# Performance work log

Hardware: AMD Instinct MI355X
Metric: run time of the kernel (lower is better)

Reference implementation:

```python
import jax, jax.numpy as jnp
import numpy as np

N_QUBITS = 16
N_LAYERS = 4
BATCH = 512


def _apply_ry(state, theta, q, n):
    # state: [B, 2^n] real (RY/CNOT circuit from |0> stays real).
    # Wire 0 is the most-significant bit (PennyLane default.qubit ordering).
    B = state.shape[0]
    pre, post = 2 ** q, 2 ** (n - q - 1)
    s = state.reshape(B, pre, 2, post)
    half = jnp.reshape(theta, (-1,)) * 0.5          # [] -> [1], [B] -> [B]
    c = jnp.cos(half)[:, None, None]
    sn = jnp.sin(half)[:, None, None]
    s0, s1 = s[:, :, 0], s[:, :, 1]
    # RY(t) = [[cos(t/2), -sin(t/2)], [sin(t/2), cos(t/2)]]
    out = jnp.stack([c * s0 - sn * s1, sn * s0 + c * s1], axis=2)
    return out.reshape(B, -1)


def _apply_cnot(state, ctrl, n):
    # CNOT with control=ctrl, target=ctrl+1 (adjacent wires).
    B = state.shape[0]
    pre, post = 2 ** ctrl, 2 ** (n - ctrl - 2)
    s = state.reshape(B, pre, 2, 2, post)
    out = jnp.stack([s[:, :, 0], s[:, :, 1, ::-1]], axis=2)
    return out.reshape(B, -1)


def setup_inputs() -> dict:
    key = jax.random.key(0)
    kx, kw = jax.random.split(key)
    x = jax.random.normal(kx, (BATCH, N_QUBITS), dtype=jnp.float32)
    weights = jax.random.normal(kw, (N_LAYERS, N_QUBITS), dtype=jnp.float32)
    return {"x": x, "weights": weights}


def reference(x, weights):
    n, L = N_QUBITS, N_LAYERS
    B = x.shape[0]
    # |0...0> initial state, batched
    state = jnp.zeros((B, 2 ** n), dtype=x.dtype).at[:, 0].set(1.0)
    # angle encoding: RY(inputs[i]) on wire i (per-sample angles)
    for i in range(n):
        state = _apply_ry(state, x[:, i], i, n)
    # variational layers: RY(weights[l, i]) then CNOT chain
    for l in range(L):
        for i in range(n):
            state = _apply_ry(state, weights[l, i], i, n)
        for i in range(n - 1):
            state = _apply_cnot(state, i, n)
    # tf.cast(complex->float32) takes the real part; state is already real.
    # Keep the first n_qubits amplitudes.
    return state[:, :n]
```

## Files before the change

### kernel.cpp

```cpp
#include <hip/hip_runtime.h>


__device__ __constant__ unsigned char WM[4][4] = {
  {0x1,0x2,0x4,0x8},{0x1,0x3,0x6,0xC},{0x1,0x2,0x5,0xA},{0x1,0x3,0x7,0xF}};
__device__ __constant__ unsigned char WS[4][4] = {
  {0x1,0x2,0x4,0x8},{0xF,0xE,0xC,0x8},{0x5,0xA,0x4,0x8},{0x3,0x6,0xC,0x8}};
__device__ __constant__ unsigned char LM[4][6] = {
  {0x01,0x02,0x04,0x08,0x10,0x20},
  {0x01,0x03,0x06,0x0C,0x18,0x30},
  {0x01,0x02,0x05,0x0A,0x14,0x28},
  {0x01,0x03,0x07,0x0F,0x1E,0x3C}};
__device__ __constant__ unsigned char LS[4][6] = {
  {0x01,0x02,0x04,0x08,0x10,0x20},
  {0x3F,0x3E,0x3C,0x38,0x30,0x20},
  {0x15,0x2A,0x14,0x28,0x10,0x20},
  {0x33,0x26,0x0C,0x18,0x30,0x20}};
__device__ __constant__ unsigned char WC[4]   = {0xF,0x5,0x3,0x1};
__device__ __constant__ unsigned char TM11[4] = {0x20,0x30,0x28,0x3C};
__device__ __constant__ unsigned char LC[4]   = {0x3F,0x15,0x33,0x11};

static constexpr int AQ[32] = {
  16,17,19,18,22,23,21,20,28,29,31,30,26,27,25,24,
   8, 9,11,10,14,15,13,12, 4, 5, 7, 6, 2, 3, 1, 0};
static constexpr int CHI[32] = {
  21,20,23,22,16,17,18,19,31,30,29,28,26,27,24,25,
   0, 1, 2, 3, 5, 4, 7, 6,10,11, 8, 9,15,14,13,12};

__global__ __launch_bounds__(1024)
void qsim_kernel(const float* __restrict__ x, const float* __restrict__ wts,
                 float* __restrict__ out) {
  __shared__ float  Lbuf[16][64][34];
  __shared__ float2 ang[80];

  const int tid   = threadIdx.x;
  const int lane  = tid & 63;
  const int wv    = tid >> 6;
  const int batch = blockIdx.x;

  if (tid < 80) {
    float th = (tid < 16) ? x[batch * 16 + tid] : wts[tid - 16];
    float s, c;
    sincosf(0.5f * th, &s, &c);
    ang[tid] = make_float2(c, s);
  }
  __syncthreads();

  float st[32];
  float2* Lf2 = (float2*)&Lbuf[wv][lane][0];

  {
    float f = 1.0f;
#pragma unroll
    for (int b = 0; b < 4; ++b) { float2 a = ang[3 - b]; f *= ((wv   >> b) & 1) ? a.y : a.x; }
#pragma unroll
    for (int e = 0; e < 6; ++e) { float2 a = ang[9 - e]; f *= ((lane >> e) & 1) ? a.y : a.x; }
    st[0] = f;
#pragma unroll
    for (int k = 0; k < 5; ++k) {
      float2 a = ang[15 - k];
      const int m = 1 << k;
#pragma unroll
      for (int r = 0; r < 16; ++r) if (r < m) {
        st[r + m] = st[r] * a.y;
        st[r]     = st[r] * a.x;
      }
    }
    float2 a10 = ang[10];
#pragma unroll
    for (int p = 0; p < 16; ++p) {
      Lf2[p] = make_float2(st[2*p] * a10.y, st[2*p+1] * a10.y);
      st[2*p] *= a10.x; st[2*p+1] *= a10.x;
    }
  }

  for (int l = 0; l < 4; ++l) {
    const float2* la = &ang[16 + l * 16];

#pragma unroll
    for (int c = 0; c < 2; ++c) {
      float t[16];
#pragma unroll
      for (int p = 0; p < 8; ++p) { float2 v = Lf2[8*c + p]; t[2*p] = v.x; t[2*p+1] = v.y; }
#pragma unroll
      for (int k = 0; k < 4; ++k) {
        const float2 a = la[15 - k];
        const int m = 1 << k;
#pragma unroll
        for (int r = 0; r < 16; ++r) if (!(r & m)) {
          float u0 = t[r], u1 = t[r + m];
          t[r]     = a.x*u0 - a.y*u1;
          t[r + m] = a.y*u0 + a.x*u1;
          float v0 = st[16*c + r], v1 = st[16*c + r + m];
          st[16*c + r]     = a.x*v0 - a.y*v1;
          st[16*c + r + m] = a.y*v0 + a.x*v1;
        }
      }
      { const float2 a5 = la[10];
#pragma unroll
        for (int j = 0; j < 16; ++j) {
          float v0 = st[16*c + j], v1 = t[j];
          st[16*c + j] = a5.x*v0 - a5.y*v1;
          t[j]         = a5.y*v0 + a5.x*v1;
        } }
#pragma unroll
      for (int p = 0; p < 8; ++p) Lf2[8*c + p] = make_float2(t[2*p], t[2*p+1]);
    }
    { const float2 a = la[11];
#pragma unroll
      for (int r = 0; r < 16; ++r) {
        float v0 = st[r], v1 = st[r + 16];
        st[r]      = a.x*v0 - a.y*v1;
        st[r + 16] = a.y*v0 + a.x*v1;
      }
#pragma unroll
      for (int p = 0; p < 8; ++p) {
        float2 A = Lf2[p], B = Lf2[p + 8];
        Lf2[p]     = make_float2(a.x*A.x - a.y*B.x, a.x*A.y - a.y*B.y);
        Lf2[p + 8] = make_float2(a.y*A.x + a.x*B.x, a.y*A.y + a.x*B.y);
      } }

    for (int e = 0; e < 6; ++e) {
      const float2 a = la[9 - e];
      const int m = LM[l][e];
      const float sg = (__popc(lane & LS[l][e]) & 1) ? a.y : -a.y;
#pragma unroll
      for (int r = 0; r < 32; ++r) {
        float o = __shfl_xor(st[r], m);
        st[r] = fmaf(sg, o, a.x * st[r]);
      }
      const float2* Pf2 = (const float2*)&Lbuf[wv][lane ^ m][0];
#pragma unroll
      for (int p = 0; p < 16; ++p) {
        float2 own = Lf2[p], oth = Pf2[p];
        Lf2[p] = make_float2(fmaf(sg, oth.x, a.x*own.x),
                             fmaf(sg, oth.y, a.x*own.y));
      }
    }

#pragma unroll
    for (int round = 0; round < 2; ++round) {
      for (int b = 0; b < 4; ++b) {
        __syncthreads();
        const float2 a = la[3 - b];
        const int m  = WM[l][b];
        const int pw = wv ^ m;
        const float sgS = (__popc(wv & WS[l][b]) & 1) ? a.y : -a.y;
        float2* P = (float2*)&Lbuf[pw][lane][0];
        const int pb = (wv < pw) ? 0 : 8;
#pragma unroll
        for (int q = 0; q < 8; ++q) {
          float2 vS = Lf2[pb + q], vP = P[pb + q];
          Lf2[pb + q] = make_float2(a.x*vS.x + sgS*vP.x, a.x*vS.y + sgS*vP.y);
          P[pb + q]   = make_float2(a.x*vP.x - sgS*vS.x, a.x*vP.y - sgS*vS.y);
        }
      }
      __syncthreads();
      if (round == 0) {
#pragma unroll
        for (int p = 0; p < 16; ++p) {
          float2 r = Lf2[p];
          Lf2[p] = make_float2(st[2*p], st[2*p+1]);
          st[2*p] = r.x; st[2*p+1] = r.y;
        }
      } else {
        float* Lrow = &Lbuf[wv][lane][0];
#pragma unroll
        for (int q = 0; q < 32; ++q) {
          float r = Lrow[q];
          Lrow[q] = st[AQ[q]];
          st[AQ[q]] = r;
        }
        float ns[32];
#pragma unroll
        for (int i = 0; i < 32; ++i) ns[CHI[i]] = st[i];
#pragma unroll
        for (int i = 0; i < 32; ++i) st[i] = ns[i];
      }
    }

    { const int tm = TM11[l];
      if (__popc(wv & WC[l]) & 1) {
#pragma unroll
        for (int r = 0; r < 32; ++r) st[r] = __shfl_xor(st[r], tm);
        const float2* Pf2 = (const float2*)&Lbuf[wv][lane ^ tm][0];
#pragma unroll
        for (int p = 0; p < 16; ++p) { float2 v = Pf2[p]; Lf2[p] = v; }
      } }
    { if (__popc(lane & LC[l]) & 1) {
#pragma unroll
        for (int p = 0; p < 16; ++p) {
          float2 v = Lf2[p ^ 15];
          Lf2[p ^ 15] = make_float2(st[2*p+1], st[2*p]);
          st[2*p] = v.y; st[2*p+1] = v.x;
        }
      } }
  }

  if (tid == 0) {
#pragma unroll
    for (int j = 0; j < 16; ++j) out[batch * 16 + j] = st[j];
  }
}

extern "C" void kernel_launch(void* const* d_in, const int* in_sizes, int n_in,
                              void* d_out, int out_size, void* d_ws, size_t ws_size,
                              hipStream_t stream) {
  const float* x   = (const float*)d_in[0];
  const float* wts = (const float*)d_in[1];
  float* out = (float*)d_out;
  const int batch = in_sizes[0] / 16;
  qsim_kernel<<<dim3(batch), dim3(1024), 0, stream>>>(x, wts, out);
}
```

Before: 303.4 us.

## Apply wave-index qubit rotations as in-register 16-point butterflies with one barrier per round

The cross-wave RY gates, which did four barrier-separated pairwise exchanges through shared memory, are replaced by a transposed pass. Each thread loads one slot across all 16 waves, applies all four rotations in registers, and writes back with a Gray-code permutation (SIG) that folds in the CNOT-induced basis change. This removes three barriers per round. The lane-qubit rotations now happen in registers via shuffles on both halves before the LDS store, instead of touching the shared-memory half through LDS reads. Other parts change to match: the AQ swap goes through float2, and the WC-based condition becomes wv&1. There is some risk of LDS bank conflicts in the strided column access and of higher register pressure.

```diff
diff --git a/kernel.cpp b/kernel.cpp
--- a/kernel.cpp
+++ b/kernel.cpp
@@ -1,10 +1,6 @@
 #include <hip/hip_runtime.h>
 
 
-__device__ __constant__ unsigned char WM[4][4] = {
-  {0x1,0x2,0x4,0x8},{0x1,0x3,0x6,0xC},{0x1,0x2,0x5,0xA},{0x1,0x3,0x7,0xF}};
-__device__ __constant__ unsigned char WS[4][4] = {
-  {0x1,0x2,0x4,0x8},{0xF,0xE,0xC,0x8},{0x5,0xA,0x4,0x8},{0x3,0x6,0xC,0x8}};
 __device__ __constant__ unsigned char LM[4][6] = {
   {0x01,0x02,0x04,0x08,0x10,0x20},
   {0x01,0x03,0x06,0x0C,0x18,0x30},
@@ -15,10 +11,10 @@
   {0x3F,0x3E,0x3C,0x38,0x30,0x20},
   {0x15,0x2A,0x14,0x28,0x10,0x20},
   {0x33,0x26,0x0C,0x18,0x30,0x20}};
-__device__ __constant__ unsigned char WC[4]   = {0xF,0x5,0x3,0x1};
 __device__ __constant__ unsigned char TM11[4] = {0x20,0x30,0x28,0x3C};
 __device__ __constant__ unsigned char LC[4]   = {0x3F,0x15,0x33,0x11};
 
+static constexpr int SIG[16] = {0,1,3,2,6,7,5,4,12,13,15,14,10,11,9,8};
 static constexpr int AQ[32] = {
   16,17,19,18,22,23,21,20,28,29,31,30,26,27,25,24,
    8, 9,11,10,14,15,13,12, 4, 5, 7, 6, 2, 3, 1, 0};
@@ -102,6 +98,18 @@
           st[16*c + j] = a5.x*v0 - a5.y*v1;
           t[j]         = a5.y*v0 + a5.x*v1;
         } }
+      for (int e = 0; e < 6; ++e) {
+        const float2 a = la[9 - e];
+        const int m = LM[l][e];
+        const float sg = (__popc(lane & LS[l][e]) & 1) ? a.y : -a.y;
+#pragma unroll
+        for (int j = 0; j < 16; ++j) {
+          float o = __shfl_xor(t[j], m);
+          t[j] = fmaf(sg, o, a.x * t[j]);
+          float o2 = __shfl_xor(st[16*c + j], m);
+          st[16*c + j] = fmaf(sg, o2, a.x * st[16*c + j]);
+        }
+      }
 #pragma unroll
       for (int p = 0; p < 8; ++p) Lf2[8*c + p] = make_float2(t[2*p], t[2*p+1]);
     }
@@ -119,40 +127,29 @@
         Lf2[p + 8] = make_float2(a.y*A.x + a.x*B.x, a.y*A.y + a.x*B.y);
       } }
 
-    for (int e = 0; e < 6; ++e) {
-      const float2 a = la[9 - e];
-      const int m = LM[l][e];
-      const float sg = (__popc(lane & LS[l][e]) & 1) ? a.y : -a.y;
-#pragma unroll
-      for (int r = 0; r < 32; ++r) {
-        float o = __shfl_xor(st[r], m);
-        st[r] = fmaf(sg, o, a.x * st[r]);
-      }
-      const float2* Pf2 = (const float2*)&Lbuf[wv][lane ^ m][0];
-#pragma unroll
-      for (int p = 0; p < 16; ++p) {
-        float2 own = Lf2[p], oth = Pf2[p];
-        Lf2[p] = make_float2(fmaf(sg, oth.x, a.x*own.x),
-                             fmaf(sg, oth.y, a.x*own.y));
-      }
-    }
-
 #pragma unroll
     for (int round = 0; round < 2; ++round) {
-      for (int b = 0; b < 4; ++b) {
-        __syncthreads();
-        const float2 a = la[3 - b];
-        const int m  = WM[l][b];
-        const int pw = wv ^ m;
-        const float sgS = (__popc(wv & WS[l][b]) & 1) ? a.y : -a.y;
-        float2* P = (float2*)&Lbuf[pw][lane][0];
-        const int pb = (wv < pw) ? 0 : 8;
-#pragma unroll
-        for (int q = 0; q < 8; ++q) {
-          float2 vS = Lf2[pb + q], vP = P[pb + q];
-          Lf2[pb + q] = make_float2(a.x*vS.x + sgS*vP.x, a.x*vS.y + sgS*vP.y);
-          P[pb + q]   = make_float2(a.x*vP.x - sgS*vS.x, a.x*vP.y - sgS*vS.y);
-        }
+      __syncthreads();
+#pragma unroll
+      for (int sl = 0; sl < 2; ++sl) {
+        const int slot = 2*wv + sl;
+        float rr[16];
+#pragma unroll
+        for (int w = 0; w < 16; ++w) rr[w] = Lbuf[w][lane][slot];
+#pragma unroll
+        for (int b = 0; b < 4; ++b) {
+          const float2 a = la[3 - b];
+          const int m = 1 << b;
+#pragma unroll
+          for (int w = 0; w < 16; ++w) if (!(w & m)) {
+            float lo = rr[w], hi = rr[w + m];
+            rr[w]     = a.x*lo - a.y*hi;
+            rr[w + m] = a.y*lo + a.x*hi;
+          }
+        }
+#pragma unroll
+        for (int w = 0; w < 16; ++w)
+          Lbuf[w][lane][slot] = rr[SIG[w]];
       }
       __syncthreads();
       if (round == 0) {
@@ -163,12 +160,11 @@
           st[2*p] = r.x; st[2*p+1] = r.y;
         }
       } else {
-        float* Lrow = &Lbuf[wv][lane][0];
-#pragma unroll
-        for (int q = 0; q < 32; ++q) {
-          float r = Lrow[q];
-          Lrow[q] = st[AQ[q]];
-          st[AQ[q]] = r;
+#pragma unroll
+        for (int p = 0; p < 16; ++p) {
+          float2 r = Lf2[p];
+          Lf2[p] = make_float2(st[AQ[2*p]], st[AQ[2*p+1]]);
+          st[AQ[2*p]] = r.x; st[AQ[2*p+1]] = r.y;
         }
         float ns[32];
 #pragma unroll
@@ -179,7 +175,7 @@
     }
 
     { const int tm = TM11[l];
-      if (__popc(wv & WC[l]) & 1) {
+      if (wv & 1) {
 #pragma unroll
         for (int r = 0; r < 32; ++r) st[r] = __shfl_xor(st[r], tm);
         const float2* Pf2 = (const float2*)&Lbuf[wv][lane ^ tm][0];
```

Measured after the change: 335.2 us. 1.1x slower.
